# Kernel optimization log

Hardware: AMD Instinct MI355X
Metric: run time of the kernel (lower is better)

Reference implementation:

```python
import jax, jax.numpy as jnp
import numpy as np

N_REV, N_USER, N_ITEM, DEG, D = 100000, 4096, 4096, 16, 64
HID = 128

def setup_inputs() -> dict:
    key = jax.random.key(0)
    ks = jax.random.split(key, 9)
    return {
        "review_vecs": jax.random.normal(ks[0], (N_REV, D), jnp.float32),
        "user_vecs": jax.random.normal(ks[1], (N_USER, D), jnp.float32),
        "item_vecs": jax.random.normal(ks[2], (N_ITEM, D), jnp.float32),
        "user_weights": jax.random.normal(ks[3], (DEG * 2 * D, HID), jnp.float32) * 0.05,
        "item_weights": jax.random.normal(ks[4], (DEG * 2 * D, HID), jnp.float32) * 0.05,
        "adj0": jax.random.randint(ks[5], (N_USER, DEG), 0, N_REV, jnp.int32),
        "adj1": jax.random.randint(ks[6], (N_USER, DEG), 0, N_ITEM, jnp.int32),
        "adj2": jax.random.randint(ks[7], (N_ITEM, DEG), 0, N_REV, jnp.int32),
        "adj3": jax.random.randint(ks[8], (N_ITEM, DEG), 0, N_USER, jnp.int32),
    }

def _sdpa(q, k, v):
    # dense scaled dot-product attention: q,k [N,d], v [N,F]
    scale = 1.0 / jnp.sqrt(jnp.asarray(q.shape[-1], q.dtype))
    w = jax.nn.softmax(jnp.einsum('nd,md->nm', q, k) * scale, axis=-1)
    return jnp.einsum('nm,mf->nf', w, v)

def reference(review_vecs, user_vecs, item_vecs, user_weights, item_weights,
              adj0, adj1, adj2, adj3):
    # dropout=0.0 -> identity; feature-dim shuffle is random augmentation,
    # replaced by identity permutation for a deterministic reference.
    ur = review_vecs[adj0]           # [Nu, deg, D]
    ri = item_vecs[adj1]             # [Nu, deg, D]
    ir = review_vecs[adj2]           # [Ni, deg, D]
    ru = user_vecs[adj3]             # [Ni, deg, D]
    cu = jnp.concatenate([ur, ri], axis=2).reshape(adj0.shape[0], -1)  # [Nu, deg*2D]
    ci = jnp.concatenate([ir, ru], axis=2).reshape(adj2.shape[0], -1)  # [Ni, deg*2D]
    cu = _sdpa(user_vecs, user_vecs, cu)
    ci = _sdpa(item_vecs, item_vecs, ci)
    user_out = jax.nn.relu(cu @ user_weights)   # [Nu, HID]
    item_out = jax.nn.relu(ci @ item_weights)   # [Ni, HID]
    return user_out, item_out
```

## Files before the change

### kernel.cpp

```cpp
#include <hip/hip_runtime.h>
#include <hip/hip_bf16.h>
#include <math.h>

#define N_NODES 4096
#define N_REV 100000
#define DEG 16
#define DIM 64
#define HID 128

typedef __attribute__((ext_vector_type(8))) short bf16x8;
typedef __attribute__((ext_vector_type(4))) float f32x4;

static __device__ __forceinline__ unsigned pk2(float a, float b) {
    __hip_bfloat162 h = __float22bfloat162_rn(make_float2(a, b));
    return *reinterpret_cast<unsigned*>(&h);
}

static __device__ __forceinline__ void gl_lds16(const void* g, void* l) {
    __builtin_amdgcn_global_load_lds(
        (const __attribute__((address_space(1))) unsigned int*)g,
        (__attribute__((address_space(3))) unsigned int*)l, 16, 0, 0);
}

__global__ __launch_bounds__(256)
void prep_vecs(const float* __restrict__ U, const float* __restrict__ I,
               ushort* __restrict__ Ub, ushort* __restrict__ Ib)
{
    int i = blockIdx.x * 256 + threadIdx.x;
    const float* src; ushort* dst; int j;
    if (i < 32768) { src = U; dst = Ub; j = i; }
    else           { src = I; dst = Ib; j = i - 32768; }
    float4 a = ((const float4*)src)[j * 2];
    float4 b = ((const float4*)src)[j * 2 + 1];
    uint4 o;
    o.x = pk2(a.x, a.y); o.y = pk2(a.z, a.w);
    o.z = pk2(b.x, b.y); o.w = pk2(b.z, b.w);
    ((uint4*)dst)[j] = o;
}

__global__ __launch_bounds__(256)
void prep_w_kernel(const float* __restrict__ uW, const float* __restrict__ iW,
                   ushort* __restrict__ wt)
{
    const int side = blockIdx.x >> 5, kc = blockIdx.x & 31;
    const float* __restrict__ W = side ? iW : uW;
    __shared__ float wt_f[64 * 128];
    const int t = threadIdx.x;
    const float4* src = (const float4*)(W + (size_t)kc * 64 * 128);
    #pragma unroll
    for (int j = 0; j < 8; ++j)
        ((float4*)wt_f)[j * 256 + t] = src[j * 256 + t];
    __syncthreads();
    #pragma unroll
    for (int j = 0; j < 4; ++j) {
        int c = j * 256 + t;
        int h = c >> 3, seg = c & 7;
        int sp = seg ^ (h & 7);
        float v[8];
        #pragma unroll
        for (int jj = 0; jj < 8; ++jj) v[jj] = wt_f[(sp * 8 + jj) * 128 + h];
        uint4 o;
        o.x = pk2(v[0], v[1]); o.y = pk2(v[2], v[3]);
        o.z = pk2(v[4], v[5]); o.w = pk2(v[6], v[7]);
        *(uint4*)(wt + ((size_t)(side * 32 + kc) * 1024 + c) * 8) = o;
    }
}

#define GB_STRIDE 16384
#define GADJ_OFF  32768

__global__ __launch_bounds__(256)
void gemm_gather(const float* __restrict__ review,
                 const float* __restrict__ userv,
                 const float* __restrict__ itemv,
                 const ushort* __restrict__ wt,
                 const int* __restrict__ adj0, const int* __restrict__ adj1,
                 const int* __restrict__ adj2, const int* __restrict__ adj3,
                 ushort* __restrict__ vprojT)
{
    const int side = blockIdx.x >> 8, rem = blockIdx.x & 255;
    const int tile = rem >> 1, hb = rem & 1;
    const int* __restrict__ adjA = side ? adj2 : adj0;
    const int* __restrict__ adjB = side ? adj3 : adj1;
    const float* __restrict__ vecB = side ? userv : itemv;
    const ushort* __restrict__ wbase = wt + (size_t)side * 32 * 8192;
    ushort* __restrict__ outT = vprojT + (size_t)side * HID * N_NODES;

    __shared__ __align__(16) char smem[36864];
    int* adjs = (int*)(smem + GADJ_OFF);
    const int t = threadIdx.x;
    const int w = t >> 6, lane = t & 63;
    const int wm = w >> 1, wn = w & 1;
    const int g = lane >> 4, qi = lane & 15;
    const int swz = (qi & 7) << 4;

    if (t < 128)
        ((int4*)adjs)[t] = ((const int4*)(adjA + tile * 512))[t];
    else
        ((int4*)adjs)[t] = ((const int4*)(adjB + tile * 512))[t - 128];
    __syncthreads();

    f32x4 acc[2];
    #pragma unroll
    for (int i = 0; i < 2; ++i) acc[i] = f32x4{0.f, 0.f, 0.f, 0.f};

    auto stage = [&](int kc, int b) {
        const int d = kc >> 1, half = kc & 1;
        char* base = smem + b * GB_STRIDE;
        const float* vs = half ? vecB : review;
        #pragma unroll
        for (int j = 0; j < 2; ++j) {
            int c = j * 256 + t;
            int row = c >> 4, seg = c & 15;
            int idx = adjs[half * 512 + row * 16 + d];
            gl_lds16(vs + (size_t)idx * 64 + (seg ^ (row & 7)) * 4,
                     base + (c >> 6) * 1024);
        }
        const ushort* wsrc = wbase + (size_t)kc * 8192;
        #pragma unroll
        for (int j = 0; j < 2; ++j) {
            int c = j * 256 + t;
            gl_lds16(wsrc + (size_t)(hb * 512 + c) * 8,
                     base + 8192 + (c >> 6) * 1024);
        }
    };

    stage(0, 0);
    __syncthreads();

    for (int kc = 0; kc < 32; ++kc) {
        const int cur = kc & 1;
        if (kc < 31) stage(kc + 1, cur ^ 1);

        const char* cb = smem + cur * GB_STRIDE;
        const int ab0 = (wm * 16 + qi) * 256 + g * 32;
        f32x4 af0 = *(const f32x4*)(cb + ((ab0)       ^ swz));
        f32x4 af1 = *(const f32x4*)(cb + ((ab0 + 16)  ^ swz));
        f32x4 af2 = *(const f32x4*)(cb + ((ab0 + 128) ^ swz));
        f32x4 af3 = *(const f32x4*)(cb + ((ab0 + 144) ^ swz));
        union { unsigned u[4]; bf16x8 s; } A0, A1;
        A0.u[0] = pk2(af0[0], af0[1]); A0.u[1] = pk2(af0[2], af0[3]);
        A0.u[2] = pk2(af1[0], af1[1]); A0.u[3] = pk2(af1[2], af1[3]);
        A1.u[0] = pk2(af2[0], af2[1]); A1.u[1] = pk2(af2[2], af2[3]);
        A1.u[2] = pk2(af3[0], af3[1]); A1.u[3] = pk2(af3[2], af3[3]);

        #pragma unroll
        for (int nf = 0; nf < 2; ++nf) {
            int bbase = 8192 + (wn * 32 + nf * 16 + qi) * 128 + g * 16;
            bf16x8 b0 = *(const bf16x8*)(cb + ((bbase)      ^ swz));
            bf16x8 b1 = *(const bf16x8*)(cb + ((bbase + 64) ^ swz));
            acc[nf] = __builtin_amdgcn_mfma_f32_16x16x32_bf16(A0.s, b0, acc[nf], 0, 0, 0);
            acc[nf] = __builtin_amdgcn_mfma_f32_16x16x32_bf16(A1.s, b1, acc[nf], 0, 0, 0);
        }
        __syncthreads();
    }

    #pragma unroll
    for (int nf = 0; nf < 2; ++nf) {
        int h = hb * 64 + wn * 32 + nf * 16 + qi;
        uint2 p;
        p.x = pk2(acc[nf][0], acc[nf][1]);
        p.y = pk2(acc[nf][2], acc[nf][3]);
        *(uint2*)(outT + (size_t)h * N_NODES + tile * 32 + wm * 16 + g * 4) = p;
    }
}

__global__ __launch_bounds__(512, 2)
void flash_attn_mfma(const float* __restrict__ userv,
                     const float* __restrict__ itemv,
                     const ushort* __restrict__ Ub,
                     const ushort* __restrict__ Ib,
                     const ushort* __restrict__ vprojT,
                     ushort* __restrict__ po,
                     float* __restrict__ pl)
{
    const int side = blockIdx.x >> 7;
    const int rem  = blockIdx.x & 127;
    const int qb   = rem >> 3;
    const int kvb  = rem & 7;
    const float* __restrict__ X = side ? itemv : userv;
    const ushort* __restrict__ Xb = side ? Ib : Ub;
    const ushort* __restrict__ V = vprojT + (size_t)side * HID * N_NODES;

    __shared__ __align__(16) char smem[81920];

    const int t = threadIdx.x;
    const int w = t >> 6, lane = t & 63;
    const int g = lane >> 4, qi = lane & 15;
    const int sw = (qi & 7) << 4;
    const int q0 = qb * 256 + w * 32;

    bf16x8 qf[2][2];
    #pragma unroll
    for (int qg = 0; qg < 2; ++qg) {
        const float* qp = X + (size_t)(q0 + qg * 16 + qi) * DIM + g * 8;
        #pragma unroll
        for (int c = 0; c < 2; ++c) {
            float4 v0 = *(const float4*)(qp + c * 32);
            float4 v1 = *(const float4*)(qp + c * 32 + 4);
            union { unsigned u[4]; bf16x8 s; } rr;
            rr.u[0] = pk2(v0.x * 0.125f, v0.y * 0.125f);
            rr.u[1] = pk2(v0.z * 0.125f, v0.w * 0.125f);
            rr.u[2] = pk2(v1.x * 0.125f, v1.y * 0.125f);
            rr.u[3] = pk2(v1.z * 0.125f, v1.w * 0.125f);
            qf[qg][c] = rr.s;
        }
    }

    f32x4 o[2][8];
    #pragma unroll
    for (int qg = 0; qg < 2; ++qg)
        #pragma unroll
        for (int ht = 0; ht < 8; ++ht) o[qg][ht] = f32x4{0.f, 0.f, 0.f, 0.f};
    float psum[2] = {0.f, 0.f};

    char* P = smem + 49152 + w * 4096;

    auto stage = [&](int it, int b) {
        const int k0 = kvb * 512 + it * 64;
        char* base = smem + b * 24576;
        {
            int row = t >> 3, seg = t & 7;
            gl_lds16(Xb + (size_t)(k0 + row) * 64 + (seg ^ (row & 7)) * 8,
                     base + (t >> 6) * 1024);
        }
        #pragma unroll
        for (int j = 0; j < 2; ++j) {
            int c = j * 512 + t;
            int hh = c >> 3, seg = c & 7;
            gl_lds16(V + (size_t)hh * N_NODES + k0 + (seg ^ (hh & 7)) * 8,
                     base + 8192 + (c >> 6) * 1024);
        }
    };

    stage(0, 0);
    __syncthreads();

    for (int it = 0; it < 8; ++it) {
        const int cur = it & 1;
        if (it < 7) stage(it + 1, cur ^ 1);
        const char* kb = smem + cur * 24576;
        const char* vt = kb + 8192;

        #pragma unroll
        for (int kt = 0; kt < 4; ++kt) {
            int abase = (kt * 16 + qi) * 128 + g * 16;
            bf16x8 ka0 = *(const bf16x8*)(kb + ((abase)      ^ sw));
            bf16x8 ka1 = *(const bf16x8*)(kb + ((abase + 64) ^ sw));
            #pragma unroll
            for (int qg = 0; qg < 2; ++qg) {
                f32x4 s = f32x4{0.f, 0.f, 0.f, 0.f};
                s = __builtin_amdgcn_mfma_f32_16x16x32_bf16(ka0, qf[qg][0], s, 0, 0, 0);
                s = __builtin_amdgcn_mfma_f32_16x16x32_bf16(ka1, qf[qg][1], s, 0, 0, 0);
                float p0 = __expf(s[0]);
                float p1 = __expf(s[1]);
                float p2 = __expf(s[2]);
                float p3 = __expf(s[3]);
                psum[qg] += (p0 + p1) + (p2 + p3);
                uint2 pr; pr.x = pk2(p0, p1); pr.y = pk2(p2, p3);
                int q = qg * 16 + qi;
                *(uint2*)(P + ((q * 128 + kt * 32 + g * 8) ^ sw)) = pr;
            }
        }

        bf16x8 pa0[2], pa1[2];
        #pragma unroll
        for (int qg = 0; qg < 2; ++qg) {
            int q = qg * 16 + qi;
            pa0[qg] = *(const bf16x8*)(P + ((q * 128 + g * 16)      ^ sw));
            pa1[qg] = *(const bf16x8*)(P + ((q * 128 + g * 16 + 64) ^ sw));
        }
        #pragma unroll
        for (int ht = 0; ht < 8; ++ht) {
            int vbase = (ht * 16 + qi) * 128 + g * 16;
            bf16x8 b0 = *(const bf16x8*)(vt + ((vbase)      ^ sw));
            bf16x8 b1 = *(const bf16x8*)(vt + ((vbase + 64) ^ sw));
            o[0][ht] = __builtin_amdgcn_mfma_f32_16x16x32_bf16(pa0[0], b0, o[0][ht], 0, 0, 0);
            o[0][ht] = __builtin_amdgcn_mfma_f32_16x16x32_bf16(pa1[0], b1, o[0][ht], 0, 0, 0);
            o[1][ht] = __builtin_amdgcn_mfma_f32_16x16x32_bf16(pa0[1], b0, o[1][ht], 0, 0, 0);
            o[1][ht] = __builtin_amdgcn_mfma_f32_16x16x32_bf16(pa1[1], b1, o[1][ht], 0, 0, 0);
        }
        __syncthreads();
    }

    #pragma unroll
    for (int qg = 0; qg < 2; ++qg) {
        psum[qg] += __shfl_xor(psum[qg], 16);
        psum[qg] += __shfl_xor(psum[qg], 32);
    }
    const int part = side * 8 + kvb;
    if (lane < 16) {
        pl[(size_t)part * N_NODES + q0 + qi]      = psum[0];
        pl[(size_t)part * N_NODES + q0 + 16 + qi] = psum[1];
    }
    ushort* pob = po + (size_t)part * N_NODES * HID;
    #pragma unroll
    for (int qg = 0; qg < 2; ++qg)
        #pragma unroll
        for (int ht = 0; ht < 8; ++ht)
            #pragma unroll
            for (int r = 0; r < 4; ++r) {
                int q = q0 + qg * 16 + 4 * g + r;
                pob[(size_t)q * HID + ht * 16 + qi] =
                    (ushort)(pk2(o[qg][ht][r], 0.f) & 0xffffu);
            }
}

__global__ __launch_bounds__(256)
void merge_parts(const ushort* __restrict__ po, const float* __restrict__ pl,
                 float* __restrict__ out)
{
    int idx = blockIdx.x * 256 + threadIdx.x;
    int side = idx >> 18;
    int q    = (idx >> 6) & 4095;
    int h2   = idx & 63;
    float sx = 0.f, sy = 0.f, l = 0.f;
    #pragma unroll
    for (int p = 0; p < 8; ++p) {
        int part = side * 8 + p;
        unsigned v = *(const unsigned*)(po + (size_t)part * (N_NODES * HID)
                                           + q * HID + h2 * 2);
        union { unsigned u; float f; } lo, hi;
        lo.u = v << 16; hi.u = v & 0xffff0000u;
        sx += lo.f; sy += hi.f;
        l += pl[(size_t)part * N_NODES + q];
    }
    float li = 1.0f / l;
    float2 r = make_float2(fmaxf(sx * li, 0.f), fmaxf(sy * li, 0.f));
    ((float2*)out)[idx] = r;
}

extern "C" void kernel_launch(void* const* d_in, const int* in_sizes, int n_in,
                              void* d_out, int out_size, void* d_ws, size_t ws_size,
                              hipStream_t stream)
{
    const float* review = (const float*)d_in[0];
    const float* userv  = (const float*)d_in[1];
    const float* itemv  = (const float*)d_in[2];
    const float* uW     = (const float*)d_in[3];
    const float* iW     = (const float*)d_in[4];
    const int*   adj0   = (const int*)d_in[5];
    const int*   adj1   = (const int*)d_in[6];
    const int*   adj2   = (const int*)d_in[7];
    const int*   adj3   = (const int*)d_in[8];
    float* out = (float*)d_out;

    char* ws = (char*)d_ws;
    char* ob = (char*)d_out;
    float*  pl     = (float*)ws;
    ushort* po     = (ushort*)(ws + 262144);
    ushort* wt     = (ushort*)(ws + 262144);
    ushort* vprojT = (ushort*)(ob);
    ushort* Ub     = (ushort*)(ob + 2097152);
    ushort* Ib     = (ushort*)(ob + 2621440);

    prep_vecs<<<256, 256, 0, stream>>>(userv, itemv, Ub, Ib);
    prep_w_kernel<<<64, 256, 0, stream>>>(uW, iW, wt);
    gemm_gather<<<512, 256, 0, stream>>>(review, userv, itemv, wt,
                                         adj0, adj1, adj2, adj3, vprojT);
    flash_attn_mfma<<<256, 512, 0, stream>>>(userv, itemv, Ub, Ib, vprojT,
                                             po, pl);
    merge_parts<<<2048, 256, 0, stream>>>(po, pl, out);
}
```

Before: 61.80 us.

## Switch flash attention to 32x32 MFMA with register-resident P via permlane swap

Rewrites the attention kernel to use 32x32x16 bf16 MFMA tiles, keeping the softmax numerators in registers and rearranging them into the A-operand layout with v_permlane32_swap rather than round-tripping through LDS. Blocks drop to 256 threads with 128 queries each, doubling the grid, and LDS shrinks since the per-wave P buffer is removed. It also merges the two prep kernels into a single launch. The aim is to cut LDS traffic and launch overhead, at the cost of relying on the MI355-specific permlane instruction and a higher accumulator register footprint.

```diff
diff --git a/kernel.cpp b/kernel.cpp
--- a/kernel.cpp
+++ b/kernel.cpp
@@ -10,6 +10,7 @@
 
 typedef __attribute__((ext_vector_type(8))) short bf16x8;
 typedef __attribute__((ext_vector_type(4))) float f32x4;
+typedef __attribute__((ext_vector_type(16))) float f32x16;
 
 static __device__ __forceinline__ unsigned pk2(float a, float b) {
     __hip_bfloat162 h = __float22bfloat162_rn(make_float2(a, b));
@@ -23,29 +24,29 @@
 }
 
 __global__ __launch_bounds__(256)
-void prep_vecs(const float* __restrict__ U, const float* __restrict__ I,
-               ushort* __restrict__ Ub, ushort* __restrict__ Ib)
-{
-    int i = blockIdx.x * 256 + threadIdx.x;
-    const float* src; ushort* dst; int j;
-    if (i < 32768) { src = U; dst = Ub; j = i; }
-    else           { src = I; dst = Ib; j = i - 32768; }
-    float4 a = ((const float4*)src)[j * 2];
-    float4 b = ((const float4*)src)[j * 2 + 1];
-    uint4 o;
-    o.x = pk2(a.x, a.y); o.y = pk2(a.z, a.w);
-    o.z = pk2(b.x, b.y); o.w = pk2(b.z, b.w);
-    ((uint4*)dst)[j] = o;
-}
-
-__global__ __launch_bounds__(256)
-void prep_w_kernel(const float* __restrict__ uW, const float* __restrict__ iW,
-                   ushort* __restrict__ wt)
-{
-    const int side = blockIdx.x >> 5, kc = blockIdx.x & 31;
-    const float* __restrict__ W = side ? iW : uW;
+void prep_all(const float* __restrict__ U, const float* __restrict__ I,
+              const float* __restrict__ uW, const float* __restrict__ iW,
+              ushort* __restrict__ Ub, ushort* __restrict__ Ib,
+              ushort* __restrict__ wt)
+{
     __shared__ float wt_f[64 * 128];
     const int t = threadIdx.x;
+    if (blockIdx.x < 256) {
+        int i = blockIdx.x * 256 + t;
+        const float* src; ushort* dst; int j;
+        if (i < 32768) { src = U; dst = Ub; j = i; }
+        else           { src = I; dst = Ib; j = i - 32768; }
+        float4 a = ((const float4*)src)[j * 2];
+        float4 b = ((const float4*)src)[j * 2 + 1];
+        uint4 o;
+        o.x = pk2(a.x, a.y); o.y = pk2(a.z, a.w);
+        o.z = pk2(b.x, b.y); o.w = pk2(b.z, b.w);
+        ((uint4*)dst)[j] = o;
+        return;
+    }
+    const int b = blockIdx.x - 256;
+    const int side = b >> 5, kc = b & 31;
+    const float* __restrict__ W = side ? iW : uW;
     const float4* src = (const float4*)(W + (size_t)kc * 64 * 128);
     #pragma unroll
     for (int j = 0; j < 8; ++j)
@@ -165,7 +166,9 @@
     }
 }
 
-__global__ __launch_bounds__(512, 2)
+#define FSTRIDE 24576
+
+__global__ __launch_bounds__(256, 2)
 void flash_attn_mfma(const float* __restrict__ userv,
                      const float* __restrict__ itemv,
                      const ushort* __restrict__ Ub,
@@ -174,59 +177,59 @@
                      ushort* __restrict__ po,
                      float* __restrict__ pl)
 {
-    const int side = blockIdx.x >> 7;
-    const int rem  = blockIdx.x & 127;
+    const int side = blockIdx.x >> 8;
+    const int rem  = blockIdx.x & 255;
     const int qb   = rem >> 3;
     const int kvb  = rem & 7;
     const float* __restrict__ X = side ? itemv : userv;
     const ushort* __restrict__ Xb = side ? Ib : Ub;
     const ushort* __restrict__ V = vprojT + (size_t)side * HID * N_NODES;
-
-    __shared__ __align__(16) char smem[81920];
+    const int part = side * 8 + kvb;
+
+    __shared__ __align__(16) char smem[49152];
 
     const int t = threadIdx.x;
     const int w = t >> 6, lane = t & 63;
-    const int g = lane >> 4, qi = lane & 15;
-    const int sw = (qi & 7) << 4;
-    const int q0 = qb * 256 + w * 32;
-
-    bf16x8 qf[2][2];
-    #pragma unroll
-    for (int qg = 0; qg < 2; ++qg) {
-        const float* qp = X + (size_t)(q0 + qg * 16 + qi) * DIM + g * 8;
-        #pragma unroll
-        for (int c = 0; c < 2; ++c) {
-            float4 v0 = *(const float4*)(qp + c * 32);
-            float4 v1 = *(const float4*)(qp + c * 32 + 4);
+    const int col = lane & 31, h5 = lane >> 5;
+    const int q0 = qb * 128 + w * 32;
+
+    bf16x8 qf[4];
+    {
+        const float* qp = X + (size_t)(q0 + col) * DIM;
+        #pragma unroll
+        for (int ks = 0; ks < 4; ++ks) {
+            int d0 = ks * 16 + h5 * 8;
+            float4 v0 = *(const float4*)(qp + d0);
+            float4 v1 = *(const float4*)(qp + d0 + 4);
             union { unsigned u[4]; bf16x8 s; } rr;
             rr.u[0] = pk2(v0.x * 0.125f, v0.y * 0.125f);
             rr.u[1] = pk2(v0.z * 0.125f, v0.w * 0.125f);
             rr.u[2] = pk2(v1.x * 0.125f, v1.y * 0.125f);
             rr.u[3] = pk2(v1.z * 0.125f, v1.w * 0.125f);
-            qf[qg][c] = rr.s;
-        }
-    }
-
-    f32x4 o[2][8];
-    #pragma unroll
-    for (int qg = 0; qg < 2; ++qg)
-        #pragma unroll
-        for (int ht = 0; ht < 8; ++ht) o[qg][ht] = f32x4{0.f, 0.f, 0.f, 0.f};
-    float psum[2] = {0.f, 0.f};
-
-    char* P = smem + 49152 + w * 4096;
+            qf[ks] = rr.s;
+        }
+    }
+
+    const f32x16 z16 = {0.f,0.f,0.f,0.f, 0.f,0.f,0.f,0.f,
+                        0.f,0.f,0.f,0.f, 0.f,0.f,0.f,0.f};
+    f32x16 o[4];
+    #pragma unroll
+    for (int ht = 0; ht < 4; ++ht) o[ht] = z16;
+    float psum = 0.f;
 
     auto stage = [&](int it, int b) {
         const int k0 = kvb * 512 + it * 64;
-        char* base = smem + b * 24576;
-        {
-            int row = t >> 3, seg = t & 7;
+        char* base = smem + b * FSTRIDE;
+        #pragma unroll
+        for (int j = 0; j < 2; ++j) {
+            int c = j * 256 + t;
+            int row = c >> 3, seg = c & 7;
             gl_lds16(Xb + (size_t)(k0 + row) * 64 + (seg ^ (row & 7)) * 8,
-                     base + (t >> 6) * 1024);
-        }
-        #pragma unroll
-        for (int j = 0; j < 2; ++j) {
-            int c = j * 512 + t;
+                     base + (c >> 6) * 1024);
+        }
+        #pragma unroll
+        for (int j = 0; j < 4; ++j) {
+            int c = j * 256 + t;
             int hh = c >> 3, seg = c & 7;
             gl_lds16(V + (size_t)hh * N_NODES + k0 + (seg ^ (hh & 7)) * 8,
                      base + 8192 + (c >> 6) * 1024);
@@ -239,71 +242,63 @@
     for (int it = 0; it < 8; ++it) {
         const int cur = it & 1;
         if (it < 7) stage(it + 1, cur ^ 1);
-        const char* kb = smem + cur * 24576;
+        const char* kb = smem + cur * FSTRIDE;
         const char* vt = kb + 8192;
 
         #pragma unroll
-        for (int kt = 0; kt < 4; ++kt) {
-            int abase = (kt * 16 + qi) * 128 + g * 16;
-            bf16x8 ka0 = *(const bf16x8*)(kb + ((abase)      ^ sw));
-            bf16x8 ka1 = *(const bf16x8*)(kb + ((abase + 64) ^ sw));
+        for (int T = 0; T < 2; ++T) {
+            f32x16 s = z16;
             #pragma unroll
-            for (int qg = 0; qg < 2; ++qg) {
-                f32x4 s = f32x4{0.f, 0.f, 0.f, 0.f};
-                s = __builtin_amdgcn_mfma_f32_16x16x32_bf16(ka0, qf[qg][0], s, 0, 0, 0);
-                s = __builtin_amdgcn_mfma_f32_16x16x32_bf16(ka1, qf[qg][1], s, 0, 0, 0);
-                float p0 = __expf(s[0]);
-                float p1 = __expf(s[1]);
-                float p2 = __expf(s[2]);
-                float p3 = __expf(s[3]);
-                psum[qg] += (p0 + p1) + (p2 + p3);
-                uint2 pr; pr.x = pk2(p0, p1); pr.y = pk2(p2, p3);
-                int q = qg * 16 + qi;
-                *(uint2*)(P + ((q * 128 + kt * 32 + g * 8) ^ sw)) = pr;
+            for (int ks = 0; ks < 4; ++ks) {
+                int row = T * 32 + col;
+                int abase = (row * 128 + ks * 32 + h5 * 16) ^ ((row & 7) << 4);
+                bf16x8 ka = *(const bf16x8*)(kb + abase);
+                s = __builtin_amdgcn_mfma_f32_32x32x16_bf16(ka, qf[ks], s, 0, 0, 0);
             }
-        }
-
-        bf16x8 pa0[2], pa1[2];
-        #pragma unroll
-        for (int qg = 0; qg < 2; ++qg) {
-            int q = qg * 16 + qi;
-            pa0[qg] = *(const bf16x8*)(P + ((q * 128 + g * 16)      ^ sw));
-            pa1[qg] = *(const bf16x8*)(P + ((q * 128 + g * 16 + 64) ^ sw));
-        }
-        #pragma unroll
-        for (int ht = 0; ht < 8; ++ht) {
-            int vbase = (ht * 16 + qi) * 128 + g * 16;
-            bf16x8 b0 = *(const bf16x8*)(vt + ((vbase)      ^ sw));
-            bf16x8 b1 = *(const bf16x8*)(vt + ((vbase + 64) ^ sw));
-            o[0][ht] = __builtin_amdgcn_mfma_f32_16x16x32_bf16(pa0[0], b0, o[0][ht], 0, 0, 0);
-            o[0][ht] = __builtin_amdgcn_mfma_f32_16x16x32_bf16(pa1[0], b1, o[0][ht], 0, 0, 0);
-            o[1][ht] = __builtin_amdgcn_mfma_f32_16x16x32_bf16(pa0[1], b0, o[1][ht], 0, 0, 0);
-            o[1][ht] = __builtin_amdgcn_mfma_f32_16x16x32_bf16(pa1[1], b1, o[1][ht], 0, 0, 0);
+            float p[16];
+            #pragma unroll
+            for (int r = 0; r < 16; ++r) {
+                p[r] = __expf(s[r]);
+                psum += p[r];
+            }
+            #pragma unroll
+            for (int win = 0; win < 2; ++win) {
+                unsigned ca0 = pk2(p[win*8 + 0], p[win*8 + 1]);
+                unsigned ca1 = pk2(p[win*8 + 2], p[win*8 + 3]);
+                unsigned cb0 = pk2(p[win*8 + 4], p[win*8 + 5]);
+                unsigned cb1 = pk2(p[win*8 + 6], p[win*8 + 7]);
+                asm volatile("v_permlane32_swap_b32 %0, %1"
+                             : "+v"(ca0), "+v"(cb0));
+                asm volatile("v_permlane32_swap_b32 %0, %1"
+                             : "+v"(ca1), "+v"(cb1));
+                union { unsigned u[4]; bf16x8 s8; } pa;
+                pa.u[0] = ca0; pa.u[1] = ca1; pa.u[2] = cb0; pa.u[3] = cb1;
+                #pragma unroll
+                for (int ht = 0; ht < 4; ++ht) {
+                    int hrow = ht * 32 + col;
+                    int vbase = (hrow * 128 + T * 64 + win * 32 + h5 * 16)
+                                ^ ((hrow & 7) << 4);
+                    bf16x8 vb = *(const bf16x8*)(vt + vbase);
+                    o[ht] = __builtin_amdgcn_mfma_f32_32x32x16_bf16(pa.s8, vb, o[ht], 0, 0, 0);
+                }
+            }
         }
         __syncthreads();
     }
 
-    #pragma unroll
-    for (int qg = 0; qg < 2; ++qg) {
-        psum[qg] += __shfl_xor(psum[qg], 16);
-        psum[qg] += __shfl_xor(psum[qg], 32);
-    }
-    const int part = side * 8 + kvb;
-    if (lane < 16) {
-        pl[(size_t)part * N_NODES + q0 + qi]      = psum[0];
-        pl[(size_t)part * N_NODES + q0 + 16 + qi] = psum[1];
-    }
+    float pt = psum + __shfl_xor(psum, 32);
+    if (lane < 32)
+        pl[(size_t)part * N_NODES + q0 + col] = pt;
+
     ushort* pob = po + (size_t)part * N_NODES * HID;
     #pragma unroll
-    for (int qg = 0; qg < 2; ++qg)
-        #pragma unroll
-        for (int ht = 0; ht < 8; ++ht)
-            #pragma unroll
-            for (int r = 0; r < 4; ++r) {
-                int q = q0 + qg * 16 + 4 * g + r;
-                pob[(size_t)q * HID + ht * 16 + qi] =
-                    (ushort)(pk2(o[qg][ht][r], 0.f) & 0xffffu);
-            }
+    for (int ht = 0; ht < 4; ++ht)
+        #pragma unroll
+        for (int r = 0; r < 16; ++r) {
+            int q = q0 + (r & 3) + 8 * (r >> 2) + 4 * h5;
+            pob[(size_t)q * HID + ht * 32 + col] =
+                (ushort)(pk2(o[ht][r], 0.f) & 0xffffu);
+        }
 }
 
 __global__ __launch_bounds__(256)
@@ -354,11 +349,10 @@
     ushort* Ub     = (ushort*)(ob + 2097152);
     ushort* Ib     = (ushort*)(ob + 2621440);
 
-    prep_vecs<<<256, 256, 0, stream>>>(userv, itemv, Ub, Ib);
-    prep_w_kernel<<<64, 256, 0, stream>>>(uW, iW, wt);
+    prep_all<<<320, 256, 0, stream>>>(userv, itemv, uW, iW, Ub, Ib, wt);
     gemm_gather<<<512, 256, 0, stream>>>(review, userv, itemv, wt,
                                          adj0, adj1, adj2, adj3, vprojT);
-    flash_attn_mfma<<<256, 512, 0, stream>>>(userv, itemv, Ub, Ib, vprojT,
+    flash_attn_mfma<<<512, 256, 0, stream>>>(userv, itemv, Ub, Ib, vprojT,
                                              po, pl);
     merge_parts<<<2048, 256, 0, stream>>>(po, pl, out);
 }
```

New measurement: 56.64 us. -8.3%, faster.
